# Kernel optimization log

Hardware: AMD Instinct MI355X
Metric: run time of the kernel (lower is better)

## Reference

```python
import jax, jax.numpy as jnp
import numpy as np

H = 8       # num_heads
HD = 32     # transformer_head_dim
LN_EPS = 1e-5


def _layernorm(x, g, b):
    m = jnp.mean(x, axis=-1, keepdims=True)
    v = jnp.mean(jnp.square(x - m), axis=-1, keepdims=True)
    return (x - m) * jax.lax.rsqrt(v + LN_EPS) * g + b


def setup_inputs() -> dict:
    key = jax.random.key(0)
    ks = jax.random.split(key, 8)
    D, DFF = 256, 1024
    B, N = 8, 2048
    s = 0.02  # weight init scale
    return {
        "x": jax.random.normal(ks[0], (B, N, D), jnp.float32),
        "w_qkv": jax.random.normal(ks[1], (3 * H * HD, D), jnp.float32) * s,
        "w_out": jax.random.normal(ks[2], (D, H * HD), jnp.float32) * s,
        "b_out": jnp.zeros((D,), jnp.float32),
        "w1": jax.random.normal(ks[3], (DFF, D), jnp.float32) * s,
        "wv": jax.random.normal(ks[4], (DFF, D), jnp.float32) * s,
        "w2": jax.random.normal(ks[5], (D, DFF), jnp.float32) * s,
        "ln1_g": jnp.ones((D,), jnp.float32),
        "ln1_b": jnp.zeros((D,), jnp.float32),
        "ln2_g": jnp.ones((D,), jnp.float32),
        "ln2_b": jnp.zeros((D,), jnp.float32),
    }


def reference(x, w_qkv, w_out, b_out, w1, wv, w2, ln1_g, ln1_b, ln2_g, ln2_b):
    B, N, D = x.shape
    scale = HD ** (-0.5)
    # --- MultiHeadedAttention ---
    qkv = x @ w_qkv.T                                   # [B,N,3*H*HD]
    q, k, v = jnp.split(qkv, 3, axis=-1)
    def to_heads(t):
        return t.reshape(B, N, H, HD).transpose(0, 2, 1, 3)  # [B,H,N,HD]
    q, k, v = to_heads(q), to_heads(k), to_heads(v)
    sim = jnp.einsum("bhid,bhjd->bhij", q, k) * scale   # [B,H,N,N]
    attn = jax.nn.softmax(sim, axis=-1)
    o = jnp.einsum("bhij,bhjd->bhid", attn, v)
    o = o.transpose(0, 2, 1, 3).reshape(B, N, H * HD)
    y = o @ w_out.T + b_out                             # attn output
    # --- attn AddNorm: ln(dropout(y)+x), dropout off ---
    x1 = _layernorm(y + x, ln1_g, ln1_b)
    # --- GEGLU FFN applied to y (faithful to source) ---
    ff = jax.nn.gelu(y @ w1.T, approximate=False) * (y @ wv.T)
    ff = ff @ w2.T
    # --- ff AddNorm ---
    return _layernorm(ff + x1, ln2_g, ln2_b)
```

## Files before the change

### kernel.cpp

```cpp
#include <hip/hip_runtime.h>

typedef unsigned short u16;
typedef __bf16 bf16;
typedef __bf16 bf16x8 __attribute__((ext_vector_type(8)));
typedef float f32x4 __attribute__((ext_vector_type(4)));
typedef unsigned short u16x8 __attribute__((ext_vector_type(8)));
typedef unsigned short u16x4 __attribute__((ext_vector_type(4)));
typedef unsigned short u16x2 __attribute__((ext_vector_type(2)));

#define DEVI static __device__ __forceinline__

DEVI float bf2f(u16 h) { return __builtin_bit_cast(float, (unsigned)h << 16); }
DEVI u16 cvt_bf(float f) { return __builtin_bit_cast(u16, (bf16)f); }

DEVI void gload16(const u16* g, u16* l) {
  __builtin_amdgcn_global_load_lds(
      (const __attribute__((address_space(1))) void*)g,
      (__attribute__((address_space(3))) void*)l, 16, 0, 0);
}

__global__ __launch_bounds__(256) void k_cast(const float* __restrict__ x,
                                              const float* __restrict__ wqkv,
                                              const float* __restrict__ wout,
                                              const float* __restrict__ w1,
                                              const float* __restrict__ wv,
                                              const float* __restrict__ w2,
                                              u16* __restrict__ dst0) {
  long i = (long)blockIdx.x * 256 + threadIdx.x;
  const float* src;
  u16* dst;
  long off;
  if (i < 1048576)       { src = x;    dst = dst0;           off = i; }
  else if (i < 1097728)  { src = wqkv; dst = dst0 + 4194304; off = i - 1048576; }
  else if (i < 1114112)  { src = wout; dst = dst0 + 4390912; off = i - 1097728; }
  else if (i < 1179648)  { src = w1;   dst = dst0 + 4456448; off = i - 1114112; }
  else if (i < 1245184)  { src = wv;   dst = dst0 + 4718592; off = i - 1179648; }
  else                   { src = w2;   dst = dst0 + 4980736; off = i - 1245184; }
  float4 f = reinterpret_cast<const float4*>(src)[off];
  u16x4 o;
  o[0] = cvt_bf(f.x); o[1] = cvt_bf(f.y); o[2] = cvt_bf(f.z); o[3] = cvt_bf(f.w);
  reinterpret_cast<u16x4*>(dst)[off] = o;
}

template <int BM, int BN, int NI>
__global__ __launch_bounds__(256) void k_gemm(const u16* __restrict__ A, const u16* __restrict__ B0,
                                              const u16* __restrict__ B1, int Nsplit,
                                              const float* __restrict__ bias,
                                              u16* __restrict__ C, int N, int K) {
  constexpr int MI = BM / 32;
  __shared__ u16 Alds[BM * 64];
  __shared__ u16 Blds[BN * 64];
  const int m0 = blockIdx.x * BM;
  const int n0 = blockIdx.y * BN;
  const u16* Ap = A + (long)m0 * K;
  const u16* Bp = (n0 < Nsplit) ? (B0 + (long)n0 * K) : (B1 + (long)(n0 - Nsplit) * K);
  const int tid = threadIdx.x, lane = tid & 63, wave = tid >> 6;
  const int wr = (wave >> 1) * (BM / 2), wc = (wave & 1) * (BN / 2);
  const int lr = lane & 15, g = lane >> 4;
  const int sr = lane >> 3, sg = lane & 7;

  f32x4 acc[MI][NI] = {};
  const int nk = K >> 6;
  for (int kt = 0; kt < nk; ++kt) {
    const int kb = kt << 6;
    __syncthreads();
#pragma unroll
    for (int c = 0; c < BM / 32; ++c) {
      const int row = wave * (BM / 4) + c * 8 + sr;
      gload16(Ap + (long)row * K + kb + ((sg ^ (row & 7)) << 3),
              &Alds[(wave * (BM / 4) + c * 8) << 6]);
    }
#pragma unroll
    for (int c = 0; c < BN / 32; ++c) {
      const int row = wave * (BN / 4) + c * 8 + sr;
      gload16(Bp + (long)row * K + kb + ((sg ^ ((row / NI) & 7)) << 3),
              &Blds[(wave * (BN / 4) + c * 8) << 6]);
    }
    __syncthreads();
#pragma unroll
    for (int kk = 0; kk < 2; ++kk) {
      bf16x8 av[MI], bv[NI];
#pragma unroll
      for (int i = 0; i < MI; ++i) {
        const int ra = wr + i * 16 + lr;
        av[i] = *reinterpret_cast<const bf16x8*>(&Alds[(ra << 6) + (((kk * 4 + g) ^ (ra & 7)) << 3)]);
      }
#pragma unroll
      for (int ni = 0; ni < NI; ++ni) {
        const int rb = wc + lr * NI + ni;
        bv[ni] = *reinterpret_cast<const bf16x8*>(&Blds[(rb << 6) + (((kk * 4 + g) ^ ((rb / NI) & 7)) << 3)]);
      }
#pragma unroll
      for (int mi = 0; mi < MI; ++mi)
#pragma unroll
        for (int ni = 0; ni < NI; ++ni)
          acc[mi][ni] = __builtin_amdgcn_mfma_f32_16x16x32_bf16(av[mi], bv[ni], acc[mi][ni], 0, 0, 0);
    }
  }
  const int colb = n0 + wc + lr * NI;
  float bvv[NI];
#pragma unroll
  for (int ni = 0; ni < NI; ++ni) bvv[ni] = bias ? bias[colb + ni] : 0.0f;
#pragma unroll
  for (int mi = 0; mi < MI; ++mi) {
#pragma unroll
    for (int r = 0; r < 4; ++r) {
      const long row = m0 + wr + mi * 16 + g * 4 + r;
      if constexpr (NI == 4) {
        u16x4 v;
#pragma unroll
        for (int ni = 0; ni < 4; ++ni) v[ni] = cvt_bf(acc[mi][ni][r] + bvv[ni]);
        *reinterpret_cast<u16x4*>(C + row * N + colb) = v;
      } else {
        u16x2 v;
#pragma unroll
        for (int ni = 0; ni < 2; ++ni) v[ni] = cvt_bf(acc[mi][ni][r] + bvv[ni]);
        *reinterpret_cast<u16x2*>(C + row * N + colb) = v;
      }
    }
  }
}

__global__ __launch_bounds__(512) void k_attn(const u16* __restrict__ qkv, u16* __restrict__ o) {
  __shared__ u16 Klds[64 * 32];
  __shared__ u16 Vtlds[32 * 72];
  __shared__ u16 Plds[8 * 16 * 72];
  const int id = blockIdx.x;
  const int qt = id >> 6;
  const int bh = id & 63;
  const int b = bh >> 3, h = bh & 7;
  const int tid = threadIdx.x;
  const int wave = tid >> 6, lane = tid & 63;
  const int lq = lane & 15, g = lane >> 4;
  const int q0 = qt * 128;
  const long qrow = (long)(b * 2048 + q0 + wave * 16 + lq);
  u16x8 qraw = *reinterpret_cast<const u16x8*>(qkv + qrow * 768 + h * 32 + g * 8);
  bf16x8 qf;
#pragma unroll
  for (int j = 0; j < 8; ++j) qf[j] = (bf16)(bf2f(qraw[j]) * 0.25503486f);

  float m = -1e30f, l = 0.0f;
  f32x4 oacc[2] = {};
  const f32x4 zero = {0.0f, 0.0f, 0.0f, 0.0f};
  u16* Pw = &Plds[wave * 16 * 72];

  for (int kt = 0; kt < 32; ++kt) {
    __syncthreads();
    const long kbase = (long)(b * 2048 + kt * 64);
    if (wave < 4) {
      gload16(qkv + (kbase + wave * 16 + (lane >> 2)) * 768 + 256 + h * 32 + (lane & 3) * 8,
              &Klds[wave * 16 * 32]);
    } else {
      const int st = tid - 256;
      const int k = st >> 2, dc = (st & 3) * 8;
      u16x8 vv = *reinterpret_cast<const u16x8*>(qkv + (kbase + k) * 768 + 512 + h * 32 + dc);
#pragma unroll
      for (int j = 0; j < 8; ++j) Vtlds[(dc + j) * 72 + k] = vv[j];
    }
    __syncthreads();

    f32x4 s[4];
#pragma unroll
    for (int f = 0; f < 4; ++f) {
      bf16x8 kf = *reinterpret_cast<const bf16x8*>(&Klds[(f * 16 + lq) * 32 + g * 8]);
      s[f] = __builtin_amdgcn_mfma_f32_16x16x32_bf16(kf, qf, zero, 0, 0, 0);
    }

    float tmax = -1e30f;
#pragma unroll
    for (int f = 0; f < 4; ++f)
#pragma unroll
      for (int r = 0; r < 4; ++r) tmax = fmaxf(tmax, s[f][r]);
    tmax = fmaxf(tmax, __shfl_xor(tmax, 16));
    tmax = fmaxf(tmax, __shfl_xor(tmax, 32));
    const float mnew = fmaxf(m, tmax);
    const float alpha = exp2f(m - mnew);
    float rsum = 0.0f;
#pragma unroll
    for (int f = 0; f < 4; ++f) {
      u16x4 pk;
#pragma unroll
      for (int r = 0; r < 4; ++r) {
        const float p = exp2f(s[f][r] - mnew);
        rsum += p;
        pk[r] = cvt_bf(p);
      }
      *reinterpret_cast<u16x4*>(Pw + lq * 72 + f * 16 + g * 4) = pk;
    }
    rsum += __shfl_xor(rsum, 16);
    rsum += __shfl_xor(rsum, 32);
    l = l * alpha + rsum;
    m = mnew;
#pragma unroll
    for (int di = 0; di < 2; ++di)
#pragma unroll
      for (int r = 0; r < 4; ++r) oacc[di][r] *= alpha;

#pragma unroll
    for (int ks = 0; ks < 2; ++ks) {
      const bf16x8 pf = *reinterpret_cast<const bf16x8*>(Pw + lq * 72 + ks * 32 + g * 8);
#pragma unroll
      for (int di = 0; di < 2; ++di) {
        bf16x8 vf = *reinterpret_cast<const bf16x8*>(&Vtlds[(di * 16 + lq) * 72 + ks * 32 + g * 8]);
        oacc[di] = __builtin_amdgcn_mfma_f32_16x16x32_bf16(vf, pf, oacc[di], 0, 0, 0);
      }
    }
  }

  const float inv = 1.0f / l;
  const long orow = (long)(b * 2048 + q0 + wave * 16 + lq);
#pragma unroll
  for (int di = 0; di < 2; ++di) {
    u16x4 ov;
#pragma unroll
    for (int r = 0; r < 4; ++r) ov[r] = cvt_bf(oacc[di][r] * inv);
    *reinterpret_cast<u16x4*>(o + orow * 256 + h * 32 + di * 16 + g * 4) = ov;
  }
}

__global__ __launch_bounds__(256) void k_ln(const u16* __restrict__ yin, const float* __restrict__ xres,
                                            const float* __restrict__ gw, const float* __restrict__ bw,
                                            float* __restrict__ out) {
  const int row = blockIdx.x * 4 + (threadIdx.x >> 6);
  const int lane = threadIdx.x & 63;
  const long base = (long)row * 256 + lane * 4;
  const float4 xv = *reinterpret_cast<const float4*>(xres + base);
  const u16x4 yv = *reinterpret_cast<const u16x4*>(yin + base);
  float s0 = bf2f(yv[0]) + xv.x;
  float s1 = bf2f(yv[1]) + xv.y;
  float s2 = bf2f(yv[2]) + xv.z;
  float s3 = bf2f(yv[3]) + xv.w;
  float sum = s0 + s1 + s2 + s3;
  float sq = s0 * s0 + s1 * s1 + s2 * s2 + s3 * s3;
#pragma unroll
  for (int msk = 1; msk < 64; msk <<= 1) {
    sum += __shfl_xor(sum, msk);
    sq += __shfl_xor(sq, msk);
  }
  const float mean = sum * (1.0f / 256.0f);
  const float var = sq * (1.0f / 256.0f) - mean * mean;
  const float rstd = rsqrtf(var + 1e-5f);
  const int c = lane * 4;
  float4 ov;
  ov.x = (s0 - mean) * rstd * gw[c + 0] + bw[c + 0];
  ov.y = (s1 - mean) * rstd * gw[c + 1] + bw[c + 1];
  ov.z = (s2 - mean) * rstd * gw[c + 2] + bw[c + 2];
  ov.w = (s3 - mean) * rstd * gw[c + 3] + bw[c + 3];
  *reinterpret_cast<float4*>(out + base) = ov;
}

__global__ __launch_bounds__(256) void k_gelumul(const u16* __restrict__ gg, u16* __restrict__ ffin) {
  const long i = ((long)blockIdx.x * 256 + threadIdx.x) * 8;
  const long row = i >> 10;
  const int c = (int)(i & 1023);
  const u16* p = gg + row * 2048 + c;
  const u16x8 a = *reinterpret_cast<const u16x8*>(p);
  const u16x8 b = *reinterpret_cast<const u16x8*>(p + 1024);
  u16x8 ov;
#pragma unroll
  for (int j = 0; j < 8; ++j) {
    const float xg = bf2f(a[j]);
    const float gl = 0.5f * xg * (1.0f + erff(xg * 0.70710678118654752f));
    ov[j] = cvt_bf(gl * bf2f(b[j]));
  }
  *reinterpret_cast<u16x8*>(ffin + i) = ov;
}

extern "C" void kernel_launch(void* const* d_in, const int* in_sizes, int n_in,
                              void* d_out, int out_size, void* d_ws, size_t ws_size,
                              hipStream_t stream) {
  (void)in_sizes; (void)n_in; (void)out_size;
  if (ws_size < 136314880ULL) return;

  const float* x     = (const float*)d_in[0];
  const float* w_qkv = (const float*)d_in[1];
  const float* w_out = (const float*)d_in[2];
  const float* b_out = (const float*)d_in[3];
  const float* w1    = (const float*)d_in[4];
  const float* wv    = (const float*)d_in[5];
  const float* w2    = (const float*)d_in[6];
  const float* ln1g  = (const float*)d_in[7];
  const float* ln1b  = (const float*)d_in[8];
  const float* ln2g  = (const float*)d_in[9];
  const float* ln2b  = (const float*)d_in[10];
  float* outp = (float*)d_out;

  char* ws = (char*)d_ws;
  u16* xb    = (u16*)ws;
  u16* wqkvb = xb + 4194304;
  u16* woutb = wqkvb + 196608;
  u16* w1b   = woutb + 65536;
  u16* wvb   = w1b + 262144;
  u16* w2b   = wvb + 262144;
  u16* qkvb  = w2b + 262144;
  u16* ob    = qkvb + 12582912;
  u16* yb    = ob + 4194304;
  float* x1  = (float*)(ws + 52428800);
  u16* gg    = (u16*)(ws + 69206016);
  u16* ffin  = qkvb;
  u16* ff2   = xb;

  k_cast<<<5120, 256, 0, stream>>>(x, w_qkv, w_out, w1, wv, w2, xb);
  k_gemm<128, 128, 4><<<dim3(128, 6), 256, 0, stream>>>(xb, wqkvb, wqkvb, 1 << 30, nullptr, qkvb, 768, 256);
  k_attn<<<1024, 512, 0, stream>>>(qkvb, ob);
  k_gemm<128, 64, 2><<<dim3(128, 4), 256, 0, stream>>>(ob, woutb, woutb, 1 << 30, b_out, yb, 256, 256);
  k_ln<<<4096, 256, 0, stream>>>(yb, x, ln1g, ln1b, x1);
  k_gemm<128, 128, 4><<<dim3(128, 16), 256, 0, stream>>>(yb, w1b, wvb, 1024, nullptr, gg, 2048, 256);
  k_gelumul<<<8192, 256, 0, stream>>>(gg, ffin);
  k_gemm<128, 64, 2><<<dim3(128, 4), 256, 0, stream>>>(ffin, w2b, w2b, 1 << 30, nullptr, ff2, 256, 1024);
  k_ln<<<4096, 256, 0, stream>>>(ff2, x1, ln2g, ln2b, outp);
}
```

Before: 282.4 us.

## Fuse GEGLU into FFN GEMM and double-buffer attention with pre-transposed V

Adds a k_glu kernel that computes the W1 and Wv projections together, with interleaved B rows and a swizzled LDS layout, and applies exact GELU times gate in the epilogue. This removes the separate gelumul kernel and the round trip of the 2048-wide intermediate through global memory. The attention kernel now uses a separate k_vt pre-pass that transposes V to global memory, takes 128-key tiles with double-buffered async LDS loads, and uses XOR-swizzled K/V/P layouts to cut bank conflicts and per-iteration synchronisation. The trade-off is an extra kernel launch plus V transpose traffic, and higher register pressure in attention.

```diff
diff --git a/kernel.cpp b/kernel.cpp
--- a/kernel.cpp
+++ b/kernel.cpp
@@ -17,6 +17,10 @@
   __builtin_amdgcn_global_load_lds(
       (const __attribute__((address_space(1))) void*)g,
       (__attribute__((address_space(3))) void*)l, 16, 0, 0);
+}
+
+DEVI float gelu_exact(float x) {
+  return 0.5f * x * (1.0f + erff(x * 0.70710678118654752f));
 }
 
 __global__ __launch_bounds__(256) void k_cast(const float* __restrict__ x,
@@ -121,54 +125,134 @@
   }
 }
 
-__global__ __launch_bounds__(512) void k_attn(const u16* __restrict__ qkv, u16* __restrict__ o) {
-  __shared__ u16 Klds[64 * 32];
-  __shared__ u16 Vtlds[32 * 72];
-  __shared__ u16 Plds[8 * 16 * 72];
+__global__ __launch_bounds__(256) void k_glu(const u16* __restrict__ A, const u16* __restrict__ W1,
+                                             const u16* __restrict__ Wv, u16* __restrict__ C) {
+  constexpr int K = 256, N = 1024;
+  __shared__ u16 Alds[128 * 64];
+  __shared__ u16 Blds[64 * 64];
+  const int m0 = blockIdx.x * 128;
+  const int n0h = blockIdx.y * 32;
+  const u16* Ap = A + (long)m0 * K;
+  const int tid = threadIdx.x, lane = tid & 63, wave = tid >> 6;
+  const int lr = lane & 15, g = lane >> 4;
+  const int sr = lane >> 3, sg = lane & 7;
+
+  f32x4 acc[2][4] = {};
+  for (int kt = 0; kt < 4; ++kt) {
+    const int kb = kt << 6;
+    __syncthreads();
+#pragma unroll
+    for (int c = 0; c < 4; ++c) {
+      const int row = wave * 32 + c * 8 + sr;
+      gload16(Ap + (long)row * K + kb + ((sg ^ (row & 7)) << 3), &Alds[(wave * 32 + c * 8) << 6]);
+    }
+#pragma unroll
+    for (int c = 0; c < 2; ++c) {
+      const int row = wave * 16 + c * 8 + sr;
+      const u16* bp = (row & 1) ? Wv : W1;
+      gload16(bp + (long)(n0h + (row >> 1)) * K + kb + ((sg ^ ((row >> 2) & 7)) << 3),
+              &Blds[(wave * 16 + c * 8) << 6]);
+    }
+    __syncthreads();
+#pragma unroll
+    for (int kk = 0; kk < 2; ++kk) {
+      bf16x8 av[2], bv[4];
+#pragma unroll
+      for (int i = 0; i < 2; ++i) {
+        const int ra = wave * 32 + i * 16 + lr;
+        av[i] = *reinterpret_cast<const bf16x8*>(&Alds[(ra << 6) + (((kk * 4 + g) ^ (ra & 7)) << 3)]);
+      }
+#pragma unroll
+      for (int ni = 0; ni < 4; ++ni) {
+        const int rb = lr * 4 + ni;
+        bv[ni] = *reinterpret_cast<const bf16x8*>(&Blds[(rb << 6) + (((kk * 4 + g) ^ ((rb >> 2) & 7)) << 3)]);
+      }
+#pragma unroll
+      for (int mi = 0; mi < 2; ++mi)
+#pragma unroll
+        for (int ni = 0; ni < 4; ++ni)
+          acc[mi][ni] = __builtin_amdgcn_mfma_f32_16x16x32_bf16(av[mi], bv[ni], acc[mi][ni], 0, 0, 0);
+    }
+  }
+  const int j0 = n0h + lr * 2;
+#pragma unroll
+  for (int mi = 0; mi < 2; ++mi) {
+#pragma unroll
+    for (int r = 0; r < 4; ++r) {
+      const long row = m0 + wave * 32 + mi * 16 + g * 4 + r;
+      u16x2 v;
+      v[0] = cvt_bf(gelu_exact(acc[mi][0][r]) * acc[mi][1][r]);
+      v[1] = cvt_bf(gelu_exact(acc[mi][2][r]) * acc[mi][3][r]);
+      *reinterpret_cast<u16x2*>(C + row * N + j0) = v;
+    }
+  }
+}
+
+__global__ __launch_bounds__(256) void k_vt(const u16* __restrict__ qkv, u16* __restrict__ vt) {
+  const int bh = blockIdx.x & 63, nt = blockIdx.x >> 6;
+  const int b = bh >> 3, h = bh & 7;
+  const int wave = threadIdx.x >> 6, lane = threadIdx.x & 63;
+  const int dcol = wave * 8;
+#pragma unroll
+  for (int i = 0; i < 4; ++i) {
+    const int nn = nt * 256 + i * 64 + lane;
+    u16x8 v = *reinterpret_cast<const u16x8*>(qkv + (long)(b * 2048 + nn) * 768 + 512 + h * 32 + dcol);
+#pragma unroll
+    for (int j = 0; j < 8; ++j)
+      vt[(long)(bh * 32 + dcol + j) * 2048 + nn] = v[j];
+  }
+}
+
+__global__ __launch_bounds__(512) void k_attn(const u16* __restrict__ qkv, const u16* __restrict__ vt,
+                                              u16* __restrict__ o) {
+  __shared__ u16 Klds[2 * 4096];
+  __shared__ u16 Vlds[2 * 4096];
+  __shared__ u16 Plds[8 * 1024];
   const int id = blockIdx.x;
-  const int qt = id >> 6;
-  const int bh = id & 63;
+  const int qt = id >> 6, bh = id & 63;
   const int b = bh >> 3, h = bh & 7;
-  const int tid = threadIdx.x;
-  const int wave = tid >> 6, lane = tid & 63;
-  const int lq = lane & 15, g = lane >> 4;
-  const int q0 = qt * 128;
-  const long qrow = (long)(b * 2048 + q0 + wave * 16 + lq);
+  const int tid = threadIdx.x, wave = tid >> 6, lane = tid & 63;
+  const int lq = lane & 15, g = lane >> 4, lqh = lq & 7;
+
+  const long qrow = (long)(b * 2048 + qt * 128 + wave * 16 + lq);
   u16x8 qraw = *reinterpret_cast<const u16x8*>(qkv + qrow * 768 + h * 32 + g * 8);
   bf16x8 qf;
 #pragma unroll
   for (int j = 0; j < 8; ++j) qf[j] = (bf16)(bf2f(qraw[j]) * 0.25503486f);
+
+  const int rK = tid >> 3, gpK = tid & 7, lK = gpK ^ (rK & 7);
+  const u16* ksrc = qkv + (long)(b * 2048 + (lK >> 2) * 64 + rK) * 768 + 256 + h * 32 + (lK & 3) * 8;
+  const int dV = tid >> 4, gpV = tid & 15, lV = (gpV & 8) | ((gpV & 7) ^ (dV & 7));
+  const u16* vsrc = vt + (long)(bh * 32 + dV) * 2048 + lV * 8;
+  u16* kdst = Klds + wave * 512;
+  u16* vdst = Vlds + wave * 512;
+
+  gload16(ksrc, kdst);
+  gload16(vsrc, vdst);
 
   float m = -1e30f, l = 0.0f;
   f32x4 oacc[2] = {};
   const f32x4 zero = {0.0f, 0.0f, 0.0f, 0.0f};
-  u16* Pw = &Plds[wave * 16 * 72];
-
-  for (int kt = 0; kt < 32; ++kt) {
-    __syncthreads();
-    const long kbase = (long)(b * 2048 + kt * 64);
-    if (wave < 4) {
-      gload16(qkv + (kbase + wave * 16 + (lane >> 2)) * 768 + 256 + h * 32 + (lane & 3) * 8,
-              &Klds[wave * 16 * 32]);
-    } else {
-      const int st = tid - 256;
-      const int k = st >> 2, dc = (st & 3) * 8;
-      u16x8 vv = *reinterpret_cast<const u16x8*>(qkv + (kbase + k) * 768 + 512 + h * 32 + dc);
-#pragma unroll
-      for (int j = 0; j < 8; ++j) Vtlds[(dc + j) * 72 + k] = vv[j];
-    }
-    __syncthreads();
-
-    f32x4 s[4];
-#pragma unroll
-    for (int f = 0; f < 4; ++f) {
-      bf16x8 kf = *reinterpret_cast<const bf16x8*>(&Klds[(f * 16 + lq) * 32 + g * 8]);
+  u16* Pw = Plds + wave * 1024;
+
+  for (int kt = 0; kt < 16; ++kt) {
+    const int bo = (kt & 1) * 4096;
+    __syncthreads();
+    if (kt + 1 < 16) {
+      const int nbo = ((kt + 1) & 1) * 4096;
+      gload16(ksrc + (long)(kt + 1) * 98304, kdst + nbo);
+      gload16(vsrc + (kt + 1) * 128, vdst + nbo);
+    }
+    f32x4 s[8];
+#pragma unroll
+    for (int f = 0; f < 8; ++f) {
+      const bf16x8 kf = *reinterpret_cast<const bf16x8*>(
+          &Klds[bo + (((f & 3) * 16 + lq) << 6) + ((((f >> 2) * 4 + g) ^ lqh) << 3)]);
       s[f] = __builtin_amdgcn_mfma_f32_16x16x32_bf16(kf, qf, zero, 0, 0, 0);
     }
-
     float tmax = -1e30f;
 #pragma unroll
-    for (int f = 0; f < 4; ++f)
+    for (int f = 0; f < 8; ++f)
 #pragma unroll
       for (int r = 0; r < 4; ++r) tmax = fmaxf(tmax, s[f][r]);
     tmax = fmaxf(tmax, __shfl_xor(tmax, 16));
@@ -177,16 +261,13 @@
     const float alpha = exp2f(m - mnew);
     float rsum = 0.0f;
 #pragma unroll
-    for (int f = 0; f < 4; ++f) {
-      u16x4 pk;
+    for (int f = 0; f < 8; ++f)
 #pragma unroll
       for (int r = 0; r < 4; ++r) {
         const float p = exp2f(s[f][r] - mnew);
+        s[f][r] = p;
         rsum += p;
-        pk[r] = cvt_bf(p);
-      }
-      *reinterpret_cast<u16x4*>(Pw + lq * 72 + f * 16 + g * 4) = pk;
-    }
+      }
     rsum += __shfl_xor(rsum, 16);
     rsum += __shfl_xor(rsum, 32);
     l = l * alpha + rsum;
@@ -197,18 +278,34 @@
       for (int r = 0; r < 4; ++r) oacc[di][r] *= alpha;
 
 #pragma unroll
-    for (int ks = 0; ks < 2; ++ks) {
-      const bf16x8 pf = *reinterpret_cast<const bf16x8*>(Pw + lq * 72 + ks * 32 + g * 8);
-#pragma unroll
-      for (int di = 0; di < 2; ++di) {
-        bf16x8 vf = *reinterpret_cast<const bf16x8*>(&Vtlds[(di * 16 + lq) * 72 + ks * 32 + g * 8]);
-        oacc[di] = __builtin_amdgcn_mfma_f32_16x16x32_bf16(vf, pf, oacc[di], 0, 0, 0);
+    for (int pass = 0; pass < 2; ++pass) {
+#pragma unroll
+      for (int fi = 0; fi < 4; ++fi) {
+        const int f = pass * 4 + fi;
+        u16x4 pk;
+#pragma unroll
+        for (int r = 0; r < 4; ++r) pk[r] = cvt_bf(s[f][r]);
+        *reinterpret_cast<u16x4*>(
+            &Pw[(lq << 6) + (((fi * 2 + (g >> 1)) ^ lqh) << 3) + ((g & 1) << 2)]) = pk;
+      }
+#pragma unroll
+      for (int ks2 = 0; ks2 < 2; ++ks2) {
+        const bf16x8 pf = *reinterpret_cast<const bf16x8*>(
+            &Pw[(lq << 6) + (((ks2 * 4 + g) ^ lqh) << 3)]);
+        const int gl = (pass * 2 + ks2) * 4 + g;
+        const int gp = (gl & 8) | ((gl & 7) ^ lqh);
+#pragma unroll
+        for (int di = 0; di < 2; ++di) {
+          const bf16x8 vf = *reinterpret_cast<const bf16x8*>(
+              &Vlds[bo + (((di * 16 + lq)) << 7) + (gp << 3)]);
+          oacc[di] = __builtin_amdgcn_mfma_f32_16x16x32_bf16(vf, pf, oacc[di], 0, 0, 0);
+        }
       }
     }
   }
 
   const float inv = 1.0f / l;
-  const long orow = (long)(b * 2048 + q0 + wave * 16 + lq);
+  const long orow = (long)(b * 2048 + qt * 128 + wave * 16 + lq);
 #pragma unroll
   for (int di = 0; di < 2; ++di) {
     u16x4 ov;
@@ -249,23 +346,6 @@
   *reinterpret_cast<float4*>(out + base) = ov;
 }
 
-__global__ __launch_bounds__(256) void k_gelumul(const u16* __restrict__ gg, u16* __restrict__ ffin) {
-  const long i = ((long)blockIdx.x * 256 + threadIdx.x) * 8;
-  const long row = i >> 10;
-  const int c = (int)(i & 1023);
-  const u16* p = gg + row * 2048 + c;
-  const u16x8 a = *reinterpret_cast<const u16x8*>(p);
-  const u16x8 b = *reinterpret_cast<const u16x8*>(p + 1024);
-  u16x8 ov;
-#pragma unroll
-  for (int j = 0; j < 8; ++j) {
-    const float xg = bf2f(a[j]);
-    const float gl = 0.5f * xg * (1.0f + erff(xg * 0.70710678118654752f));
-    ov[j] = cvt_bf(gl * bf2f(b[j]));
-  }
-  *reinterpret_cast<u16x8*>(ffin + i) = ov;
-}
-
 extern "C" void kernel_launch(void* const* d_in, const int* in_sizes, int n_in,
                               void* d_out, int out_size, void* d_ws, size_t ws_size,
                               hipStream_t stream) {
@@ -296,17 +376,17 @@
   u16* ob    = qkvb + 12582912;
   u16* yb    = ob + 4194304;
   float* x1  = (float*)(ws + 52428800);
-  u16* gg    = (u16*)(ws + 69206016);
+  u16* vtb   = (u16*)(ws + 69206016);
   u16* ffin  = qkvb;
   u16* ff2   = xb;
 
   k_cast<<<5120, 256, 0, stream>>>(x, w_qkv, w_out, w1, wv, w2, xb);
   k_gemm<128, 128, 4><<<dim3(128, 6), 256, 0, stream>>>(xb, wqkvb, wqkvb, 1 << 30, nullptr, qkvb, 768, 256);
-  k_attn<<<1024, 512, 0, stream>>>(qkvb, ob);
+  k_vt<<<512, 256, 0, stream>>>(qkvb, vtb);
+  k_attn<<<1024, 512, 0, stream>>>(qkvb, vtb, ob);
   k_gemm<128, 64, 2><<<dim3(128, 4), 256, 0, stream>>>(ob, woutb, woutb, 1 << 30, b_out, yb, 256, 256);
   k_ln<<<4096, 256, 0, stream>>>(yb, x, ln1g, ln1b, x1);
-  k_gemm<128, 128, 4><<<dim3(128, 16), 256, 0, stream>>>(yb, w1b, wvb, 1024, nullptr, gg, 2048, 256);
-  k_gelumul<<<8192, 256, 0, stream>>>(gg, ffin);
+  k_glu<<<dim3(128, 32), 256, 0, stream>>>(yb, w1b, wvb, ffin);
   k_gemm<128, 64, 2><<<dim3(128, 4), 256, 0, stream>>>(ffin, w2b, w2b, 1 << 30, nullptr, ff2, 256, 1024);
   k_ln<<<4096, 256, 0, stream>>>(ff2, x1, ln2g, ln2b, outp);
 }
```

New measurement: 269.7 us. 1.05x faster.
